# Performance work log

Measured on AMD Instinct MI355X. Metric: run time of the kernel, lower is better.

Reference implementation:

```python
import jax, jax.numpy as jnp
import numpy as np

DIM = 768; HEADS = 12; DIM_HEAD = 64; INNER = HEADS * DIM_HEAD
GT_HEADS = 8; GT_DH = 64; GT_INNER = GT_HEADS * GT_DH
W = 128; DEPTH = 4; NUM_TOKENS = 32000; SEQ = 4096; MAX_SEQ = 4096; B = 1
FF_MULT = 4


def layer_norm(x, g, b, eps=1e-5):
    mu = x.mean(-1, keepdims=True)
    var = ((x - mu) ** 2).mean(-1, keepdims=True)
    return (x - mu) / jnp.sqrt(var + eps) * g + b


def ffn(x, w1_, b1_, w2_, b2_):
    return jax.nn.gelu(x @ w1_ + b1_, approximate=False) @ w2_ + b2_


def global_attn(g, wqkv, wo_, bo_):
    # full causal MHA over the (few) global tokens
    b, n, _ = g.shape
    q, k, v = jnp.split(g @ wqkv, 3, axis=-1)
    sh = lambda t: t.reshape(b, n, GT_HEADS, GT_DH).transpose(0, 2, 1, 3)  # b h n d
    q, k, v = sh(q), sh(k), sh(v)
    sim = jnp.einsum('bhid,bhjd->bhij', q, k) * (GT_DH ** -0.5)
    cm = jnp.triu(jnp.ones((n, n), dtype=bool), k=1)
    sim = jnp.where(cm, -jnp.finfo(sim.dtype).max, sim)
    attn = jax.nn.softmax(sim, axis=-1)
    out = jnp.einsum('bhij,bhjd->bhid', attn, v)
    out = out.transpose(0, 2, 1, 3).reshape(b, n, GT_INNER)
    return out @ wo_ + bo_


def local_attn(x, g, wq_, wkv_, wo_, bo_):
    # windowed look-back attention + global-token keys. n assumed multiple of W.
    b, n, _ = x.shape
    bh = b * HEADS
    buckets = n // W
    sh = lambda t, m: t.reshape(b, m, HEADS, DIM_HEAD).transpose(0, 2, 1, 3).reshape(bh, m, DIM_HEAD)
    q = sh(x @ wq_, n)
    k, v = jnp.split(x @ wkv_, 2, axis=-1)
    k, v = sh(k, n), sh(v, n)
    win = lambda t: t.reshape(bh, buckets, W, DIM_HEAD)
    q, k, v = win(q), win(k), win(v)
    kp = jnp.pad(k, ((0, 0), (1, 0), (0, 0), (0, 0)))
    # NOTE: faithfully replicates upstream bug -- the lambda in the torch code
    # builds BOTH k and v from k, so v becomes the k look-back concat too.
    k2 = jnp.concatenate([kp[:, :-1], kp[:, 1:]], axis=2)  # [bh, buckets, 2W, d]
    v2 = k2
    local_j = 2 * W
    # global tokens (last one dropped)
    gt = g[:, :-1]
    ng = gt.shape[1]
    gk, gv = jnp.split(gt @ wkv_, 2, axis=-1)
    gsh = lambda t: t.reshape(b, ng, HEADS, DIM_HEAD).transpose(0, 2, 1, 3).reshape(bh, ng, DIM_HEAD)
    gk = jnp.broadcast_to(gsh(gk)[:, None], (bh, buckets, ng, DIM_HEAD))
    gv = jnp.broadcast_to(gsh(gv)[:, None], (bh, buckets, ng, DIM_HEAD))
    kf = jnp.concatenate([gk, k2], axis=2)
    vf = jnp.concatenate([gv, v2], axis=2)
    sim = jnp.einsum('bwid,bwjd->bwij', q, kf) * (DIM_HEAD ** -0.5)
    mv = -jnp.finfo(sim.dtype).max
    m_local = jnp.triu(jnp.ones((W, local_j), dtype=bool), k=local_j - W + 1)
    m_local = jnp.broadcast_to(m_local[None], (buckets, W, local_j))
    m_glob = jnp.triu(jnp.ones((buckets, ng), dtype=bool), k=ng - W)
    m_glob = jnp.broadcast_to(m_glob[:, None, :], (buckets, W, ng))
    cmask = jnp.concatenate([m_glob, m_local], axis=-1)[None]
    sim = jnp.where(cmask, mv, sim)
    attn = jax.nn.softmax(sim, axis=-1)
    out = jnp.einsum('bwij,bwjd->bwid', attn, vf)
    out = out.reshape(b, HEADS, n, DIM_HEAD).transpose(0, 2, 1, 3).reshape(b, n, INNER)
    return out @ wo_ + bo_


def setup_inputs() -> dict:
    ks = iter(jax.random.split(jax.random.key(0), 64))
    nrm = lambda shape: jax.random.normal(next(ks), shape, jnp.float32) * 0.02
    return {
        'x': jax.random.randint(next(ks), (B, SEQ), 0, NUM_TOKENS),
        'token_emb': nrm((NUM_TOKENS, DIM)),
        'pos_emb': nrm((MAX_SEQ, DIM)),
        'global_pos_emb': nrm((MAX_SEQ // W, DIM)),
        'gt_ln1_g': jnp.ones((DIM,)), 'gt_ln1_b': jnp.zeros((DIM,)),
        'gt_wqkv': nrm((DIM, 3 * GT_INNER)), 'gt_wo': nrm((GT_INNER, DIM)), 'gt_bo': jnp.zeros((DIM,)),
        'gt_ln2_g': jnp.ones((DIM,)), 'gt_ln2_b': jnp.zeros((DIM,)),
        'gt_w1': nrm((DIM, FF_MULT * DIM)), 'gt_b1': jnp.zeros((FF_MULT * DIM,)),
        'gt_w2': nrm((FF_MULT * DIM, DIM)), 'gt_b2': jnp.zeros((DIM,)),
        'ln1_g': jnp.ones((DEPTH, DIM)), 'ln1_b': jnp.zeros((DEPTH, DIM)),
        'wq': nrm((DEPTH, DIM, INNER)), 'wkv': nrm((DEPTH, DIM, 2 * INNER)),
        'wo': nrm((DEPTH, INNER, DIM)), 'bo': jnp.zeros((DEPTH, DIM)),
        'ln2_g': jnp.ones((DEPTH, DIM)), 'ln2_b': jnp.zeros((DEPTH, DIM)),
        'w1': nrm((DEPTH, DIM, FF_MULT * DIM)), 'b1': jnp.zeros((DEPTH, FF_MULT * DIM)),
        'w2': nrm((DEPTH, FF_MULT * DIM, DIM)), 'b2': jnp.zeros((DEPTH, DIM)),
        'f_ln_g': jnp.ones((DIM,)), 'f_ln_b': jnp.zeros((DIM,)),
        'w_logits': nrm((DIM, NUM_TOKENS)), 'b_logits': jnp.zeros((NUM_TOKENS,)),
    }


def reference(x, token_emb, pos_emb, global_pos_emb,
              gt_ln1_g, gt_ln1_b, gt_wqkv, gt_wo, gt_bo,
              gt_ln2_g, gt_ln2_b, gt_w1, gt_b1, gt_w2, gt_b2,
              ln1_g, ln1_b, wq, wkv, wo, bo,
              ln2_g, ln2_b, w1, b1, w2, b2,
              f_ln_g, f_ln_b, w_logits, b_logits):
    b, n = x.shape
    buckets = n // W  # n % W == 0 for chosen shapes -> r = 0 branch
    h = token_emb[x]                                    # [b, n, dim]
    g = h.reshape(b, buckets, W, DIM).mean(axis=2)      # pooled global tokens
    h = h + pos_emb[:n][None]
    g = g + global_pos_emb[:buckets][None]
    for l in range(DEPTH):
        g = g + global_attn(layer_norm(g, gt_ln1_g, gt_ln1_b), gt_wqkv, gt_wo, gt_bo)
        g = g + ffn(layer_norm(g, gt_ln2_g, gt_ln2_b), gt_w1, gt_b1, gt_w2, gt_b2)
        h = h + local_attn(layer_norm(h, ln1_g[l], ln1_b[l]), g, wq[l], wkv[l], wo[l], bo[l])
        h = h + ffn(layer_norm(h, ln2_g[l], ln2_b[l]), w1[l], b1[l], w2[l], b2[l])
    return layer_norm(h, f_ln_g, f_ln_b) @ w_logits + b_logits
```

## Files before the change

kernel.cpp:

```cpp
#include <hip/hip_runtime.h>
#include <hip/hip_bf16.h>


#define DIMM   768
#define SEQLEN 4096
#define NHEADS 12
#define DH     64
#define WWIN   128
#define NBUCK  32
#define NDEPTH 4
#define FFDIM  3072
#define NTOK   32000
#define QKLD   1536
#define NEG_MAX (-3.402823466e38f)

typedef unsigned short u16;
typedef __attribute__((ext_vector_type(8))) short bf16x8;
typedef __attribute__((ext_vector_type(4))) float f32x4;

#define GLOAD16(gp, lp) \
  __builtin_amdgcn_global_load_lds((const __attribute__((address_space(1))) void*)(gp), \
                                   (__attribute__((address_space(3))) void*)(lp), 16, 0, 0)

__device__ __forceinline__ float b2f(u16 u) {
  union { unsigned int i; float f; } c; c.i = ((unsigned int)u) << 16; return c.f;
}

__global__ __launch_bounds__(256) void embed_kernel(
    const int* __restrict__ x, const float* __restrict__ tok,
    const float* __restrict__ pos, float* __restrict__ h) {
  int row = blockIdx.x;
  int t = threadIdx.x;
  int tk = x[row];
  const float* te = tok + (size_t)tk * DIMM;
  const float* pe = pos + (size_t)row * DIMM;
  float* hr = h + (size_t)row * DIMM;
  hr[t]       = te[t]       + pe[t];
  hr[t + 256] = te[t + 256] + pe[t + 256];
  hr[t + 512] = te[t + 512] + pe[t + 512];
}

__global__ __launch_bounds__(256) void ln_kernel(
    const float* __restrict__ in, const float* __restrict__ gam,
    const float* __restrict__ bet, __hip_bfloat16* __restrict__ out) {
  int row = blockIdx.x;
  int t = threadIdx.x;
  const float* xr = in + (size_t)row * DIMM;
  float v0 = xr[t], v1 = xr[t + 256], v2 = xr[t + 512];
  float s  = v0 + v1 + v2;
  float s2 = v0 * v0 + v1 * v1 + v2 * v2;
  #pragma unroll
  for (int o = 32; o > 0; o >>= 1) {
    s  += __shfl_down(s, o);
    s2 += __shfl_down(s2, o);
  }
  __shared__ float red[2][4];
  int wid = t >> 6, lane = t & 63;
  if (lane == 0) { red[0][wid] = s; red[1][wid] = s2; }
  __syncthreads();
  if (t == 0) {
    float ts  = red[0][0] + red[0][1] + red[0][2] + red[0][3];
    float ts2 = red[1][0] + red[1][1] + red[1][2] + red[1][3];
    float mean = ts * (1.0f / DIMM);
    float var  = ts2 * (1.0f / DIMM) - mean * mean;
    red[0][0] = mean;
    red[1][0] = rsqrtf(var + 1e-5f);
  }
  __syncthreads();
  float mean = red[0][0], rstd = red[1][0];
  __hip_bfloat16* orow = out + (size_t)row * DIMM;
  orow[t]       = __float2bfloat16((v0 - mean) * rstd * gam[t]       + bet[t]);
  orow[t + 256] = __float2bfloat16((v1 - mean) * rstd * gam[t + 256] + bet[t + 256]);
  orow[t + 512] = __float2bfloat16((v2 - mean) * rstd * gam[t + 512] + bet[t + 512]);
}

__global__ __launch_bounds__(256) void wprep_kernel(
    const float* __restrict__ src, u16* __restrict__ dst,
    int ldsrc, int Krows, size_t sls, size_t dls) {
  __shared__ float tile[32][33];
  int l = blockIdx.z;
  int n0 = blockIdx.x * 32, k0 = blockIdx.y * 32;
  int tx = threadIdx.x & 31, ty = threadIdx.x >> 5;
  const float* s = src + (size_t)l * sls;
  u16* d = dst + (size_t)l * dls;
  #pragma unroll
  for (int i = 0; i < 4; ++i)
    tile[ty + i * 8][tx] = s[(size_t)(k0 + ty + i * 8) * ldsrc + n0 + tx];
  __syncthreads();
  #pragma unroll
  for (int i = 0; i < 4; ++i) {
    __hip_bfloat16 b = __float2bfloat16(tile[tx][ty + i * 8]);
    d[(size_t)(n0 + ty + i * 8) * Krows + k0 + tx] = *(u16*)&b;
  }
}

template<int TBM>
__global__ __launch_bounds__(256) void gemm_bf16(
    const u16* __restrict__ A, const u16* __restrict__ Bt,
    const float* __restrict__ bias, const float* __restrict__ resid,
    void* __restrict__ Cv, int K, int ldc, int act, int cbf16) {
  constexpr int MFR = TBM / 32;
  __shared__ u16 As[2][TBM * 32];
  __shared__ u16 Bs[2][128 * 32];
  int tid = threadIdx.x;
  int wave = tid >> 6, lane = tid & 63;

  int lin = blockIdx.y * gridDim.x + blockIdx.x;
  int cpx = (gridDim.x * gridDim.y) >> 3;
  int swz = (lin & 7) * cpx + (lin >> 3);
  int by = swz % gridDim.y;
  int bx = swz / gridDim.y;

  int bm = by * TBM, bn = bx * 128;
  int wm = (wave >> 1) * (TBM / 2), wn = (wave & 1) * 64;
  int fr = lane & 15, fq = lane >> 4;

  f32x4 zero = {0.f, 0.f, 0.f, 0.f};
  f32x4 acc[MFR][4];
  #pragma unroll
  for (int i = 0; i < MFR; ++i)
    #pragma unroll
    for (int j = 0; j < 4; ++j) acc[i][j] = zero;

  int r0 = tid >> 2;
  int kb = ((tid & 3) ^ ((r0 >> 1) & 3)) * 8;
  const u16* aptr = A + (size_t)(bm + r0) * K + kb;
  const u16* bptr = Bt + (size_t)(bn + r0) * K + kb;
  int sA = (fq ^ ((fr >> 1) & 3)) * 8;

#define STAGE_TILE(buf) do {                                          \
    char* lA = (char*)(&As[buf][0]) + wave * 1024;                    \
    char* lB = (char*)(&Bs[buf][0]) + wave * 1024;                    \
    GLOAD16(aptr, lA);                                                \
    if constexpr (TBM == 128) GLOAD16(aptr + (size_t)64 * K, lA + 4096); \
    GLOAD16(bptr, lB);                                                \
    GLOAD16(bptr + (size_t)64 * K, lB + 4096);                        \
    aptr += 32; bptr += 32;                                           \
  } while (0)

  int nk = K >> 5;
  STAGE_TILE(0);
  __syncthreads();

  for (int t = 0; t < nk; ++t) {
    int cur = t & 1;
    if (t + 1 < nk) STAGE_TILE(cur ^ 1);
    bf16x8 af[MFR], bfr[4];
    #pragma unroll
    for (int m = 0; m < MFR; ++m)
      af[m] = *(const bf16x8*)&As[cur][(wm + m * 16 + fr) * 32 + sA];
    #pragma unroll
    for (int n = 0; n < 4; ++n)
      bfr[n] = *(const bf16x8*)&Bs[cur][(wn + n * 16 + fr) * 32 + sA];
    #pragma unroll
    for (int m = 0; m < MFR; ++m)
      #pragma unroll
      for (int n = 0; n < 4; ++n)
        acc[m][n] = __builtin_amdgcn_mfma_f32_16x16x32_bf16(af[m], bfr[n], acc[m][n], 0, 0, 0);
    __syncthreads();
  }
#undef STAGE_TILE

  #pragma unroll
  for (int m = 0; m < MFR; ++m) {
    #pragma unroll
    for (int rr = 0; rr < 4; ++rr) {
      int row = bm + wm + m * 16 + fq * 4 + rr;
      #pragma unroll
      for (int n = 0; n < 4; ++n) {
        int col = bn + wn + n * 16 + fr;
        float v = acc[m][n][rr];
        if (bias) v += bias[col];
        if (act) v = 0.5f * v * (1.0f + erff(v * 0.70710678118654752f));
        if (resid) v += resid[(size_t)row * ldc + col];
        if (cbf16) {
          __hip_bfloat16 b = __float2bfloat16(v);
          ((u16*)Cv)[(size_t)row * ldc + col] = *(u16*)&b;
        } else {
          ((float*)Cv)[(size_t)row * ldc + col] = v;
        }
      }
    }
  }
}

__global__ __launch_bounds__(512, 1) void gemm256(
    const u16* __restrict__ A, const u16* __restrict__ Bt,
    const float* __restrict__ bias, float* __restrict__ C, int K, int ldc) {
  __shared__ __align__(16) char GL[131072];
  const int tid = threadIdx.x;
  const int wave = tid >> 6, lane = tid & 63;
  const int fr = lane & 15, fq = lane >> 4;

  int lin = blockIdx.y * gridDim.x + blockIdx.x;
  int cpx = (gridDim.x * gridDim.y) >> 3;
  int swz = (lin & 7) * cpx + (lin >> 3);
  int by = swz % gridDim.y;
  int bx = swz / gridDim.y;

  const int bm = by * 256, bn = bx * 256;
  const int wm = (wave >> 2) * 128, wn = (wave & 3) * 64;

  const int r_in = tid >> 3;
  const int g_log = (tid & 7) ^ (r_in & 7);
  const size_t a_base = (size_t)(bm + r_in) * K + g_log * 8;
  const size_t b_base = (size_t)(bn + r_in) * K + g_log * 8;
  const int lds_st = wave * 1024;

  const int slot0 = ((fq) ^ (fr & 7)) * 16;
  const int slot1 = ((4 + fq) ^ (fr & 7)) * 16;

  f32x4 acc[8][4];
  #pragma unroll
  for (int i = 0; i < 8; ++i)
    #pragma unroll
    for (int j = 0; j < 4; ++j) acc[i][j] = (f32x4){0.f, 0.f, 0.f, 0.f};

  bf16x8 aq[4][2], bp0[2][2], bp1[2][2];

#define STG4(gb, ldsoff) do {                                   \
    const u16* g_ = (gb);                                       \
    GLOAD16(g_,                  GL + (ldsoff) + lds_st);       \
    GLOAD16(g_ + (size_t)64 * K,  GL + (ldsoff) + 8192 + lds_st);  \
    GLOAD16(g_ + (size_t)128 * K, GL + (ldsoff) + 16384 + lds_st); \
    GLOAD16(g_ + (size_t)192 * K, GL + (ldsoff) + 24576 + lds_st); \
  } while (0)

#define RD_AQ(QOFF, c)                                                   \
    _Pragma("unroll") for (int mm = 0; mm < 4; ++mm) {                   \
      const char* p_ = GL + (c) * 32768 + (wm + (QOFF) + mm * 16 + fr) * 128; \
      aq[mm][0] = *(const bf16x8*)(p_ + slot0);                          \
      aq[mm][1] = *(const bf16x8*)(p_ + slot1);                          \
    }
#define RD_BP(BP, NOFF, c)                                               \
    _Pragma("unroll") for (int nn = 0; nn < 2; ++nn) {                   \
      const char* p_ = GL + 65536 + (c) * 32768 + (wn + (NOFF) + nn * 16 + fr) * 128; \
      BP[nn][0] = *(const bf16x8*)(p_ + slot0);                          \
      BP[nn][1] = *(const bf16x8*)(p_ + slot1);                          \
    }
#define MMA8(MB, NB, BP)                                                 \
    _Pragma("unroll") for (int mm = 0; mm < 4; ++mm)                     \
      _Pragma("unroll") for (int nn = 0; nn < 2; ++nn)                   \
        _Pragma("unroll") for (int kk = 0; kk < 2; ++kk)                 \
          acc[(MB) + mm][(NB) + nn] = __builtin_amdgcn_mfma_f32_16x16x32_bf16( \
              aq[mm][kk], BP[nn][kk], acc[(MB) + mm][(NB) + nn], 0, 0, 0);
#define BAR()      __builtin_amdgcn_s_barrier()
#define SBAR()     __builtin_amdgcn_sched_barrier(0)
#define PRIO(x)    __builtin_amdgcn_s_setprio(x)
#define VMDRAIN()  asm volatile("s_waitcnt vmcnt(0)" ::: "memory")

  const int nk = K >> 6;
  STG4(A + a_base, 0);
  STG4(Bt + b_base, 65536);
  VMDRAIN();
  BAR();

  for (int t = 0; t < nk; ++t) {
    const int c = t & 1;
    if (t + 1 < nk) STG4(A + a_base + (size_t)(t + 1) * 64, (c ^ 1) * 32768);
    RD_AQ(0, c); RD_BP(bp0, 0, c);
    BAR();
    PRIO(1); MMA8(0, 0, bp0); PRIO(0);
    SBAR(); BAR();
    if (t + 1 < nk) STG4(Bt + b_base + (size_t)(t + 1) * 64, 65536 + (c ^ 1) * 32768);
    RD_BP(bp1, 32, c);
    BAR();
    PRIO(1); MMA8(0, 2, bp1); PRIO(0);
    SBAR(); BAR();
    RD_AQ(64, c);
    BAR();
    PRIO(1); MMA8(4, 2, bp1); PRIO(0);
    SBAR(); BAR();
    PRIO(1); MMA8(4, 0, bp0); PRIO(0);
    SBAR();
    VMDRAIN();
    BAR();
  }
#undef STG4
#undef RD_AQ
#undef RD_BP
#undef MMA8

  #pragma unroll
  for (int m = 0; m < 8; ++m) {
    #pragma unroll
    for (int rr = 0; rr < 4; ++rr) {
      int row = bm + wm + m * 16 + fq * 4 + rr;
      #pragma unroll
      for (int n = 0; n < 4; ++n) {
        int col = bn + wn + n * 16 + fr;
        C[(size_t)row * ldc + col] = acc[m][n][rr] + bias[col];
      }
    }
  }
}

__global__ __launch_bounds__(256, 1) void attn_mfma(
    const u16* __restrict__ QK, u16* __restrict__ CTX) {
  __shared__ __align__(16) char LDS[131072];
  char* Kl = LDS;
  char* Kt = LDS + 32768;
  const int w = blockIdx.x, hd = blockIdx.y;
  const int tid = threadIdx.x;
  const int wave = tid >> 6, lane = tid & 63;
  const int fr = lane & 15, fq = lane >> 4;
  char* Pw = LDS + 65536 + wave * 16384;

  {
    const int j = tid;
    const int p = (w - 1) * WWIN + j;
    bf16x8 kv[8];
    if (p >= 0) {
      const bf16x8* src = (const bf16x8*)(QK + (size_t)p * QKLD + DIMM + hd * DH);
      #pragma unroll
      for (int g = 0; g < 8; ++g) kv[g] = src[g];
    } else {
      #pragma unroll
      for (int g = 0; g < 8; ++g) kv[g] = (bf16x8){0, 0, 0, 0, 0, 0, 0, 0};
    }
    #pragma unroll
    for (int g = 0; g < 8; ++g)
      *(bf16x8*)(Kl + j * 128 + ((g ^ (j & 7)) * 16)) = kv[g];
    #pragma unroll
    for (int g = 0; g < 8; ++g)
      #pragma unroll
      for (int e = 0; e < 8; ++e) {
        const int d = g * 8 + e;
        *(u16*)(Kt + d * 512 + (((j >> 3) ^ (d & 7)) * 16) + ((j & 7) * 2)) =
            (u16)kv[g][e];
      }
  }

  bf16x8 aq[2][2];
  #pragma unroll
  for (int m = 0; m < 2; ++m)
    #pragma unroll
    for (int kk = 0; kk < 2; ++kk)
      aq[m][kk] = *(const bf16x8*)(QK +
          (size_t)(w * WWIN + wave * 32 + m * 16 + fr) * QKLD + hd * DH + kk * 32 + fq * 8);

  __syncthreads();

  f32x4 sacc[2][16];
  #pragma unroll
  for (int m = 0; m < 2; ++m)
    #pragma unroll
    for (int n = 0; n < 16; ++n) sacc[m][n] = (f32x4){0.f, 0.f, 0.f, 0.f};
  #pragma unroll
  for (int n = 0; n < 16; ++n) {
    #pragma unroll
    for (int kk = 0; kk < 2; ++kk) {
      bf16x8 bk = *(const bf16x8*)(Kl + (n * 16 + fr) * 128 +
                                   (((kk * 4 + fq) ^ (fr & 7)) * 16));
      #pragma unroll
      for (int m = 0; m < 2; ++m)
        sacc[m][n] = __builtin_amdgcn_mfma_f32_16x16x32_bf16(aq[m][kk], bk, sacc[m][n], 0, 0, 0);
    }
  }

  float inv_[2][4];
  #pragma unroll
  for (int m = 0; m < 2; ++m) {
    #pragma unroll
    for (int rr = 0; rr < 4; ++rr) {
      const int r = wave * 32 + m * 16 + fq * 4 + rr;
      float pv[16];
      float mx = NEG_MAX;
      #pragma unroll
      for (int n = 0; n < 16; ++n) {
        const int j = n * 16 + fr;
        float s = sacc[m][n][rr] * 0.125f;
        bool vis = (j <= r + 128);
        pv[n] = vis ? s : NEG_MAX;
        if (vis) mx = fmaxf(mx, s);
      }
      #pragma unroll
      for (int o = 1; o < 16; o <<= 1) mx = fmaxf(mx, __shfl_xor(mx, o));
      float sum = 0.f;
      #pragma unroll
      for (int n = 0; n < 16; ++n) {
        float p = (pv[n] != NEG_MAX) ? __expf(pv[n] - mx) : 0.f;
        pv[n] = p;
        sum += p;
      }
      #pragma unroll
      for (int o = 1; o < 16; o <<= 1) sum += __shfl_xor(sum, o);
      inv_[m][rr] = 1.0f / sum;
      const int rl = m * 16 + fq * 4 + rr;
      #pragma unroll
      for (int n = 0; n < 16; ++n) {
        __hip_bfloat16 b = __float2bfloat16(pv[n]);
        const int gj = n * 2 + (fr >> 3);
        *(u16*)(Pw + rl * 512 + ((gj ^ (rl & 7)) * 16) + ((fr & 7) * 2)) = *(u16*)&b;
      }
    }
  }
  __syncthreads();

  f32x4 oacc[2][4];
  #pragma unroll
  for (int m = 0; m < 2; ++m)
    #pragma unroll
    for (int nd = 0; nd < 4; ++nd) oacc[m][nd] = (f32x4){0.f, 0.f, 0.f, 0.f};
  #pragma unroll
  for (int kc = 0; kc < 8; ++kc) {
    const int slot = ((kc * 4 + fq) ^ (fr & 7)) * 16;
    bf16x8 pa[2];
    #pragma unroll
    for (int m = 0; m < 2; ++m)
      pa[m] = *(const bf16x8*)(Pw + (m * 16 + fr) * 512 + slot);
    #pragma unroll
    for (int nd = 0; nd < 4; ++nd) {
      bf16x8 kb = *(const bf16x8*)(Kt + (nd * 16 + fr) * 512 + slot);
      #pragma unroll
      for (int m = 0; m < 2; ++m)
        oacc[m][nd] = __builtin_amdgcn_mfma_f32_16x16x32_bf16(pa[m], kb, oacc[m][nd], 0, 0, 0);
    }
  }

  #pragma unroll
  for (int m = 0; m < 2; ++m)
    #pragma unroll
    for (int nd = 0; nd < 4; ++nd)
      #pragma unroll
      for (int rr = 0; rr < 4; ++rr) {
        const int row = w * WWIN + wave * 32 + m * 16 + fq * 4 + rr;
        const int col = hd * DH + nd * 16 + fr;
        __hip_bfloat16 b = __float2bfloat16(oacc[m][nd][rr] * inv_[m][rr]);
        CTX[(size_t)row * DIMM + col] = *(u16*)&b;
      }
}

extern "C" void kernel_launch(void* const* d_in, const int* in_sizes, int n_in,
                              void* d_out, int out_size, void* d_ws, size_t ws_size,
                              hipStream_t stream) {
  const int*   x         = (const int*)d_in[0];
  const float* token_emb = (const float*)d_in[1];
  const float* pos_emb   = (const float*)d_in[2];
  const float* ln1_g = (const float*)d_in[15];
  const float* ln1_b = (const float*)d_in[16];
  const float* wq    = (const float*)d_in[17];
  const float* wkv   = (const float*)d_in[18];
  const float* wo    = (const float*)d_in[19];
  const float* bo    = (const float*)d_in[20];
  const float* ln2_g = (const float*)d_in[21];
  const float* ln2_b = (const float*)d_in[22];
  const float* w1    = (const float*)d_in[23];
  const float* b1    = (const float*)d_in[24];
  const float* w2    = (const float*)d_in[25];
  const float* b2    = (const float*)d_in[26];
  const float* f_ln_g = (const float*)d_in[27];
  const float* f_ln_b = (const float*)d_in[28];
  const float* w_logits = (const float*)d_in[29];
  const float* b_logits = (const float*)d_in[30];
  float* out = (float*)d_out;

  char* ob = (char*)d_out;
  float* h    = (float*)(ob + 0);
  u16* qk     = (u16*)(ob + 12582912);
  u16* ctx    = (u16*)(ob + 25165824);
  u16* mid    = (u16*)(ob + 31457280);
  u16* warena = (u16*)(ob + 56623104);
  const size_t WQ_SZ = (size_t)DIMM * DIMM;
  const size_t W1_SZ = (size_t)DIMM * FFDIM;
  const size_t LW = 3 * WQ_SZ + 2 * W1_SZ;
  u16* qkw_t = warena;
  u16* wo_t  = warena + 2 * WQ_SZ;
  u16* w1_t  = warena + 3 * WQ_SZ;
  u16* w2_t  = warena + 3 * WQ_SZ + W1_SZ;

  u16* wlog_t = (u16*)d_ws;
  __hip_bfloat16* lnbuf = (__hip_bfloat16*)((char*)d_ws + 49152000);

  wprep_kernel<<<dim3(24, 24, 4), 256, 0, stream>>>(wq,  qkw_t,         DIMM,   DIMM,  WQ_SZ,   LW);
  wprep_kernel<<<dim3(24, 24, 4), 256, 0, stream>>>(wkv, qkw_t + WQ_SZ, 2*DIMM, DIMM,  2*WQ_SZ, LW);
  wprep_kernel<<<dim3(24, 24, 4), 256, 0, stream>>>(wo,  wo_t,          DIMM,   DIMM,  WQ_SZ,   LW);
  wprep_kernel<<<dim3(96, 24, 4), 256, 0, stream>>>(w1,  w1_t,          FFDIM,  DIMM,  W1_SZ,   LW);
  wprep_kernel<<<dim3(24, 96, 4), 256, 0, stream>>>(w2,  w2_t,          DIMM,   FFDIM, W1_SZ,   LW);
  wprep_kernel<<<dim3(1000, 24, 1), 256, 0, stream>>>(w_logits, wlog_t, NTOK, DIMM, 0, 0);

  embed_kernel<<<SEQLEN, 256, 0, stream>>>(x, token_emb, pos_emb, h);

  for (int l = 0; l < NDEPTH; ++l) {
    ln_kernel<<<SEQLEN, 256, 0, stream>>>(h, ln1_g + l * DIMM, ln1_b + l * DIMM, lnbuf);
    gemm_bf16<64><<<dim3(12, 64), 256, 0, stream>>>(
        (const u16*)lnbuf, qkw_t + l * LW, nullptr, nullptr, qk, DIMM, QKLD, 0, 1);
    attn_mfma<<<dim3(NBUCK, NHEADS), 256, 0, stream>>>(qk, ctx);
    gemm_bf16<64><<<dim3(6, 64), 256, 0, stream>>>(
        ctx, wo_t + l * LW, bo + l * DIMM, h, h, DIMM, DIMM, 0, 0);
    ln_kernel<<<SEQLEN, 256, 0, stream>>>(h, ln2_g + l * DIMM, ln2_b + l * DIMM, lnbuf);
    gemm_bf16<128><<<dim3(24, 32), 256, 0, stream>>>(
        (const u16*)lnbuf, w1_t + l * LW, b1 + l * FFDIM, nullptr, mid, DIMM, FFDIM, 1, 1);
    gemm_bf16<64><<<dim3(6, 64), 256, 0, stream>>>(
        mid, w2_t + l * LW, b2 + l * DIMM, h, h, FFDIM, DIMM, 0, 0);
  }

  ln_kernel<<<SEQLEN, 256, 0, stream>>>(h, f_ln_g, f_ln_b, lnbuf);
  gemm256<<<dim3(NTOK / 256, SEQLEN / 256), 512, 0, stream>>>(
      (const u16*)lnbuf, wlog_t, b_logits, out, DIMM, NTOK);
}
```

Baseline: 1.232 ms.

## Replace templated layer GEMM with 128x128 K64 pipelined MFMA kernel

Swaps the per-layer bf16 GEMM for a new 128x128-tile kernel with a 64-wide K step, XOR-swizzled LDS and double buffering. Global-to-LDS loads for the next tile are interleaved with four MFMA phases, separated by barriers and raised wave priority. The QK, out-projection and W2 GEMMs move from 64-row to 128-row tiles, halving their grid. This aims to cut LDS/barrier overhead per FLOP and overlap loads with math, at the cost of fewer blocks (192 for the N=768 GEMMs) on a large-CU GPU.

```diff
diff --git a/kernel.cpp b/kernel.cpp
--- a/kernel.cpp
+++ b/kernel.cpp
@@ -22,9 +22,10 @@
   __builtin_amdgcn_global_load_lds((const __attribute__((address_space(1))) void*)(gp), \
                                    (__attribute__((address_space(3))) void*)(lp), 16, 0, 0)
 
-__device__ __forceinline__ float b2f(u16 u) {
-  union { unsigned int i; float f; } c; c.i = ((unsigned int)u) << 16; return c.f;
-}
+#define BAR()      __builtin_amdgcn_s_barrier()
+#define SBAR()     __builtin_amdgcn_sched_barrier(0)
+#define PRIO(x)    __builtin_amdgcn_s_setprio(x)
+#define VMDRAIN()  asm volatile("s_waitcnt vmcnt(0)" ::: "memory")
 
 __global__ __launch_bounds__(256) void embed_kernel(
     const int* __restrict__ x, const float* __restrict__ tok,
@@ -94,16 +95,14 @@
   }
 }
 
-template<int TBM>
-__global__ __launch_bounds__(256) void gemm_bf16(
+__global__ __launch_bounds__(256) void gemm128d(
     const u16* __restrict__ A, const u16* __restrict__ Bt,
     const float* __restrict__ bias, const float* __restrict__ resid,
     void* __restrict__ Cv, int K, int ldc, int act, int cbf16) {
-  constexpr int MFR = TBM / 32;
-  __shared__ u16 As[2][TBM * 32];
-  __shared__ u16 Bs[2][128 * 32];
-  int tid = threadIdx.x;
-  int wave = tid >> 6, lane = tid & 63;
+  __shared__ __align__(16) char GL[65536];
+  const int tid = threadIdx.x;
+  const int wave = tid >> 6, lane = tid & 63;
+  const int fr = lane & 15, fq = lane >> 4;
 
   int lin = blockIdx.y * gridDim.x + blockIdx.x;
   int cpx = (gridDim.x * gridDim.y) >> 3;
@@ -111,58 +110,89 @@
   int by = swz % gridDim.y;
   int bx = swz / gridDim.y;
 
-  int bm = by * TBM, bn = bx * 128;
-  int wm = (wave >> 1) * (TBM / 2), wn = (wave & 1) * 64;
-  int fr = lane & 15, fq = lane >> 4;
-
-  f32x4 zero = {0.f, 0.f, 0.f, 0.f};
-  f32x4 acc[MFR][4];
-  #pragma unroll
-  for (int i = 0; i < MFR; ++i)
-    #pragma unroll
-    for (int j = 0; j < 4; ++j) acc[i][j] = zero;
-
-  int r0 = tid >> 2;
-  int kb = ((tid & 3) ^ ((r0 >> 1) & 3)) * 8;
-  const u16* aptr = A + (size_t)(bm + r0) * K + kb;
-  const u16* bptr = Bt + (size_t)(bn + r0) * K + kb;
-  int sA = (fq ^ ((fr >> 1) & 3)) * 8;
-
-#define STAGE_TILE(buf) do {                                          \
-    char* lA = (char*)(&As[buf][0]) + wave * 1024;                    \
-    char* lB = (char*)(&Bs[buf][0]) + wave * 1024;                    \
-    GLOAD16(aptr, lA);                                                \
-    if constexpr (TBM == 128) GLOAD16(aptr + (size_t)64 * K, lA + 4096); \
-    GLOAD16(bptr, lB);                                                \
-    GLOAD16(bptr + (size_t)64 * K, lB + 4096);                        \
-    aptr += 32; bptr += 32;                                           \
-  } while (0)
-
-  int nk = K >> 5;
-  STAGE_TILE(0);
-  __syncthreads();
+  const int bm = by * 128, bn = bx * 128;
+  const int wm = (wave >> 1) * 64, wn = (wave & 1) * 64;
+
+  const int r_in = tid >> 3;
+  const int g_log = (tid & 7) ^ (r_in & 7);
+  const size_t a_base = (size_t)(bm + r_in) * K + g_log * 8;
+  const size_t b_base = (size_t)(bn + r_in) * K + g_log * 8;
+  const int lds_st = wave * 1024;
+
+  const int slot0 = (fq ^ (fr & 7)) * 16;
+  const int slot1 = ((4 + fq) ^ (fr & 7)) * 16;
+
+  f32x4 acc[4][4];
+  #pragma unroll
+  for (int i = 0; i < 4; ++i)
+    #pragma unroll
+    for (int j = 0; j < 4; ++j) acc[i][j] = (f32x4){0.f, 0.f, 0.f, 0.f};
+
+  bf16x8 aq[4][2], bf0[2], bf1[2], bf2[2], bf3[2];
+
+#define STG4A(tt, c) do { const u16* g_ = A + a_base + (size_t)(tt) * 64;   \
+    GLOAD16(g_,                 GL + (c) * 16384 + lds_st);                 \
+    GLOAD16(g_ + (size_t)32 * K, GL + (c) * 16384 + 4096 + lds_st);         \
+    GLOAD16(g_ + (size_t)64 * K, GL + (c) * 16384 + 8192 + lds_st);         \
+    GLOAD16(g_ + (size_t)96 * K, GL + (c) * 16384 + 12288 + lds_st); } while (0)
+#define STG4B(tt, c) do { const u16* g_ = Bt + b_base + (size_t)(tt) * 64;  \
+    GLOAD16(g_,                 GL + 32768 + (c) * 16384 + lds_st);         \
+    GLOAD16(g_ + (size_t)32 * K, GL + 32768 + (c) * 16384 + 4096 + lds_st); \
+    GLOAD16(g_ + (size_t)64 * K, GL + 32768 + (c) * 16384 + 8192 + lds_st); \
+    GLOAD16(g_ + (size_t)96 * K, GL + 32768 + (c) * 16384 + 12288 + lds_st); } while (0)
+#define RD_A(c)                                                             \
+    _Pragma("unroll") for (int mm = 0; mm < 4; ++mm) {                      \
+      const char* p_ = GL + (c) * 16384 + (wm + mm * 16 + fr) * 128;        \
+      aq[mm][0] = *(const bf16x8*)(p_ + slot0);                             \
+      aq[mm][1] = *(const bf16x8*)(p_ + slot1);                             \
+    }
+#define RD_B(BF, NOFF, c) do {                                              \
+      const char* p_ = GL + 32768 + (c) * 16384 + (wn + (NOFF) + fr) * 128; \
+      BF[0] = *(const bf16x8*)(p_ + slot0);                                 \
+      BF[1] = *(const bf16x8*)(p_ + slot1);                                 \
+    } while (0)
+#define MMA4(N, BF)                                                         \
+    _Pragma("unroll") for (int mm = 0; mm < 4; ++mm)                        \
+      _Pragma("unroll") for (int kk = 0; kk < 2; ++kk)                      \
+        acc[mm][N] = __builtin_amdgcn_mfma_f32_16x16x32_bf16(               \
+            aq[mm][kk], BF[kk], acc[mm][N], 0, 0, 0);
+
+  const int nk = K >> 6;
+  STG4A(0, 0);
+  STG4B(0, 0);
+  VMDRAIN();
+  BAR();
 
   for (int t = 0; t < nk; ++t) {
-    int cur = t & 1;
-    if (t + 1 < nk) STAGE_TILE(cur ^ 1);
-    bf16x8 af[MFR], bfr[4];
-    #pragma unroll
-    for (int m = 0; m < MFR; ++m)
-      af[m] = *(const bf16x8*)&As[cur][(wm + m * 16 + fr) * 32 + sA];
-    #pragma unroll
-    for (int n = 0; n < 4; ++n)
-      bfr[n] = *(const bf16x8*)&Bs[cur][(wn + n * 16 + fr) * 32 + sA];
-    #pragma unroll
-    for (int m = 0; m < MFR; ++m)
-      #pragma unroll
-      for (int n = 0; n < 4; ++n)
-        acc[m][n] = __builtin_amdgcn_mfma_f32_16x16x32_bf16(af[m], bfr[n], acc[m][n], 0, 0, 0);
-    __syncthreads();
-  }
-#undef STAGE_TILE
-
-  #pragma unroll
-  for (int m = 0; m < MFR; ++m) {
+    const int c = t & 1;
+    if (t + 1 < nk) STG4A(t + 1, c ^ 1);
+    RD_A(c); RD_B(bf0, 0, c);
+    BAR();
+    PRIO(1); MMA4(0, bf0); PRIO(0);
+    SBAR(); BAR();
+    if (t + 1 < nk) STG4B(t + 1, c ^ 1);
+    RD_B(bf1, 16, c);
+    BAR();
+    PRIO(1); MMA4(1, bf1); PRIO(0);
+    SBAR(); BAR();
+    RD_B(bf2, 32, c);
+    BAR();
+    PRIO(1); MMA4(2, bf2); PRIO(0);
+    SBAR(); BAR();
+    RD_B(bf3, 48, c);
+    PRIO(1); MMA4(3, bf3); PRIO(0);
+    SBAR();
+    VMDRAIN();
+    BAR();
+  }
+#undef STG4A
+#undef STG4B
+#undef RD_A
+#undef RD_B
+#undef MMA4
+
+  #pragma unroll
+  for (int m = 0; m < 4; ++m) {
     #pragma unroll
     for (int rr = 0; rr < 4; ++rr) {
       int row = bm + wm + m * 16 + fq * 4 + rr;
@@ -244,10 +274,6 @@
         _Pragma("unroll") for (int kk = 0; kk < 2; ++kk)                 \
           acc[(MB) + mm][(NB) + nn] = __builtin_amdgcn_mfma_f32_16x16x32_bf16( \
               aq[mm][kk], BP[nn][kk], acc[(MB) + mm][(NB) + nn], 0, 0, 0);
-#define BAR()      __builtin_amdgcn_s_barrier()
-#define SBAR()     __builtin_amdgcn_sched_barrier(0)
-#define PRIO(x)    __builtin_amdgcn_s_setprio(x)
-#define VMDRAIN()  asm volatile("s_waitcnt vmcnt(0)" ::: "memory")
 
   const int nk = K >> 6;
   STG4(A + a_base, 0);
@@ -483,15 +509,15 @@
 
   for (int l = 0; l < NDEPTH; ++l) {
     ln_kernel<<<SEQLEN, 256, 0, stream>>>(h, ln1_g + l * DIMM, ln1_b + l * DIMM, lnbuf);
-    gemm_bf16<64><<<dim3(12, 64), 256, 0, stream>>>(
+    gemm128d<<<dim3(12, 32), 256, 0, stream>>>(
         (const u16*)lnbuf, qkw_t + l * LW, nullptr, nullptr, qk, DIMM, QKLD, 0, 1);
     attn_mfma<<<dim3(NBUCK, NHEADS), 256, 0, stream>>>(qk, ctx);
-    gemm_bf16<64><<<dim3(6, 64), 256, 0, stream>>>(
+    gemm128d<<<dim3(6, 32), 256, 0, stream>>>(
         ctx, wo_t + l * LW, bo + l * DIMM, h, h, DIMM, DIMM, 0, 0);
     ln_kernel<<<SEQLEN, 256, 0, stream>>>(h, ln2_g + l * DIMM, ln2_b + l * DIMM, lnbuf);
-    gemm_bf16<128><<<dim3(24, 32), 256, 0, stream>>>(
+    gemm128d<<<dim3(24, 32), 256, 0, stream>>>(
         (const u16*)lnbuf, w1_t + l * LW, b1 + l * FFDIM, nullptr, mid, DIMM, FFDIM, 1, 1);
-    gemm_bf16<64><<<dim3(6, 64), 256, 0, stream>>>(
+    gemm128d<<<dim3(6, 32), 256, 0, stream>>>(
         mid, w2_t + l * LW, b2 + l * DIMM, h, h, FFDIM, DIMM, 0, 0);
   }
 
```

New measurement: 1.381 ms. 12.2% more time.

## Deepen gemm_bf16 K-tile to 64 with XOR-swizzled LDS and larger QK tile

Applied to the files above, without the earlier changes.

The generic bf16 GEMM now stages 64-wide K slices per iteration instead of 32, using an 8-slot XOR swizzle for the LDS layout. Each barrier therefore covers twice as many MFMAs, which halves loop and synchronisation overhead. The QK projection GEMM switches from 64-row to 128-row tiles, which halves the grid and raises reuse of the B operand. The cost is double the LDS per block and more registers, which can lower occupancy, and the QK launch has fewer blocks (384).

```diff
diff --git a/kernel.cpp b/kernel.cpp
--- a/kernel.cpp
+++ b/kernel.cpp
@@ -22,9 +22,10 @@
   __builtin_amdgcn_global_load_lds((const __attribute__((address_space(1))) void*)(gp), \
                                    (__attribute__((address_space(3))) void*)(lp), 16, 0, 0)
 
-__device__ __forceinline__ float b2f(u16 u) {
-  union { unsigned int i; float f; } c; c.i = ((unsigned int)u) << 16; return c.f;
-}
+#define BAR()      __builtin_amdgcn_s_barrier()
+#define SBAR()     __builtin_amdgcn_sched_barrier(0)
+#define PRIO(x)    __builtin_amdgcn_s_setprio(x)
+#define VMDRAIN()  asm volatile("s_waitcnt vmcnt(0)" ::: "memory")
 
 __global__ __launch_bounds__(256) void embed_kernel(
     const int* __restrict__ x, const float* __restrict__ tok,
@@ -100,10 +101,11 @@
     const float* __restrict__ bias, const float* __restrict__ resid,
     void* __restrict__ Cv, int K, int ldc, int act, int cbf16) {
   constexpr int MFR = TBM / 32;
-  __shared__ u16 As[2][TBM * 32];
-  __shared__ u16 Bs[2][128 * 32];
-  int tid = threadIdx.x;
-  int wave = tid >> 6, lane = tid & 63;
+  __shared__ __align__(16) u16 As[2][TBM * 64];
+  __shared__ __align__(16) u16 Bs[2][128 * 64];
+  const int tid = threadIdx.x;
+  const int wave = tid >> 6, lane = tid & 63;
+  const int fr = lane & 15, fq = lane >> 4;
 
   int lin = blockIdx.y * gridDim.x + blockIdx.x;
   int cpx = (gridDim.x * gridDim.y) >> 3;
@@ -111,52 +113,69 @@
   int by = swz % gridDim.y;
   int bx = swz / gridDim.y;
 
-  int bm = by * TBM, bn = bx * 128;
-  int wm = (wave >> 1) * (TBM / 2), wn = (wave & 1) * 64;
-  int fr = lane & 15, fq = lane >> 4;
-
-  f32x4 zero = {0.f, 0.f, 0.f, 0.f};
+  const int bm = by * TBM, bn = bx * 128;
+  const int wm = (wave >> 1) * (TBM / 2), wn = (wave & 1) * 64;
+
   f32x4 acc[MFR][4];
   #pragma unroll
   for (int i = 0; i < MFR; ++i)
     #pragma unroll
-    for (int j = 0; j < 4; ++j) acc[i][j] = zero;
-
-  int r0 = tid >> 2;
-  int kb = ((tid & 3) ^ ((r0 >> 1) & 3)) * 8;
-  const u16* aptr = A + (size_t)(bm + r0) * K + kb;
-  const u16* bptr = Bt + (size_t)(bn + r0) * K + kb;
-  int sA = (fq ^ ((fr >> 1) & 3)) * 8;
-
-#define STAGE_TILE(buf) do {                                          \
-    char* lA = (char*)(&As[buf][0]) + wave * 1024;                    \
-    char* lB = (char*)(&Bs[buf][0]) + wave * 1024;                    \
-    GLOAD16(aptr, lA);                                                \
-    if constexpr (TBM == 128) GLOAD16(aptr + (size_t)64 * K, lA + 4096); \
-    GLOAD16(bptr, lB);                                                \
-    GLOAD16(bptr + (size_t)64 * K, lB + 4096);                        \
-    aptr += 32; bptr += 32;                                           \
+    for (int j = 0; j < 4; ++j) acc[i][j] = (f32x4){0.f, 0.f, 0.f, 0.f};
+
+  const int r_in = tid >> 3;
+  const int g_log = (tid & 7) ^ (r_in & 7);
+  const size_t a_base = (size_t)(bm + r_in) * K + g_log * 8;
+  const size_t b_base = (size_t)(bn + r_in) * K + g_log * 8;
+  const int lds_st = wave * 1024;
+
+  const int slot0 = (fq ^ (fr & 7)) * 16;
+  const int slot1 = ((4 + fq) ^ (fr & 7)) * 16;
+
+#define STAGE_TILE(tt, buf) do {                                             \
+    char* lA = (char*)(&As[buf][0]) + lds_st;                                \
+    char* lB = (char*)(&Bs[buf][0]) + lds_st;                                \
+    const u16* ga = A + a_base + (size_t)(tt) * 64;                          \
+    const u16* gb = Bt + b_base + (size_t)(tt) * 64;                         \
+    GLOAD16(ga, lA);                                                         \
+    GLOAD16(ga + (size_t)32 * K, lA + 4096);                                 \
+    if constexpr (TBM == 128) {                                              \
+      GLOAD16(ga + (size_t)64 * K, lA + 8192);                               \
+      GLOAD16(ga + (size_t)96 * K, lA + 12288);                              \
+    }                                                                        \
+    GLOAD16(gb, lB);                                                         \
+    GLOAD16(gb + (size_t)32 * K, lB + 4096);                                 \
+    GLOAD16(gb + (size_t)64 * K, lB + 8192);                                 \
+    GLOAD16(gb + (size_t)96 * K, lB + 12288);                                \
   } while (0)
 
-  int nk = K >> 5;
-  STAGE_TILE(0);
+  const int nk = K >> 6;
+  STAGE_TILE(0, 0);
   __syncthreads();
 
   for (int t = 0; t < nk; ++t) {
-    int cur = t & 1;
-    if (t + 1 < nk) STAGE_TILE(cur ^ 1);
-    bf16x8 af[MFR], bfr[4];
+    const int cur = t & 1;
+    if (t + 1 < nk) STAGE_TILE(t + 1, cur ^ 1);
+    bf16x8 af[MFR][2], bfr[4][2];
+    #pragma unroll
+    for (int m = 0; m < MFR; ++m) {
+      const char* p_ = (const char*)(&As[cur][0]) + (wm + m * 16 + fr) * 128;
+      af[m][0] = *(const bf16x8*)(p_ + slot0);
+      af[m][1] = *(const bf16x8*)(p_ + slot1);
+    }
+    #pragma unroll
+    for (int n = 0; n < 4; ++n) {
+      const char* p_ = (const char*)(&Bs[cur][0]) + (wn + n * 16 + fr) * 128;
+      bfr[n][0] = *(const bf16x8*)(p_ + slot0);
+      bfr[n][1] = *(const bf16x8*)(p_ + slot1);
+    }
     #pragma unroll
     for (int m = 0; m < MFR; ++m)
-      af[m] = *(const bf16x8*)&As[cur][(wm + m * 16 + fr) * 32 + sA];
-    #pragma unroll
-    for (int n = 0; n < 4; ++n)
-      bfr[n] = *(const bf16x8*)&Bs[cur][(wn + n * 16 + fr) * 32 + sA];
-    #pragma unroll
-    for (int m = 0; m < MFR; ++m)
       #pragma unroll
       for (int n = 0; n < 4; ++n)
-        acc[m][n] = __builtin_amdgcn_mfma_f32_16x16x32_bf16(af[m], bfr[n], acc[m][n], 0, 0, 0);
+        #pragma unroll
+        for (int kk = 0; kk < 2; ++kk)
+          acc[m][n] = __builtin_amdgcn_mfma_f32_16x16x32_bf16(
+              af[m][kk], bfr[n][kk], acc[m][n], 0, 0, 0);
     __syncthreads();
   }
 #undef STAGE_TILE
@@ -244,10 +263,6 @@
         _Pragma("unroll") for (int kk = 0; kk < 2; ++kk)                 \
           acc[(MB) + mm][(NB) + nn] = __builtin_amdgcn_mfma_f32_16x16x32_bf16( \
               aq[mm][kk], BP[nn][kk], acc[(MB) + mm][(NB) + nn], 0, 0, 0);
-#define BAR()      __builtin_amdgcn_s_barrier()
-#define SBAR()     __builtin_amdgcn_sched_barrier(0)
-#define PRIO(x)    __builtin_amdgcn_s_setprio(x)
-#define VMDRAIN()  asm volatile("s_waitcnt vmcnt(0)" ::: "memory")
 
   const int nk = K >> 6;
   STG4(A + a_base, 0);
@@ -483,7 +498,7 @@
 
   for (int l = 0; l < NDEPTH; ++l) {
     ln_kernel<<<SEQLEN, 256, 0, stream>>>(h, ln1_g + l * DIMM, ln1_b + l * DIMM, lnbuf);
-    gemm_bf16<64><<<dim3(12, 64), 256, 0, stream>>>(
+    gemm_bf16<128><<<dim3(12, 32), 256, 0, stream>>>(
         (const u16*)lnbuf, qkw_t + l * LW, nullptr, nullptr, qk, DIMM, QKLD, 0, 1);
     attn_mfma<<<dim3(NBUCK, NHEADS), 256, 0, stream>>>(qk, ctx);
     gemm_bf16<64><<<dim3(6, 64), 256, 0, stream>>>(
```

Result: slower. 1.324 ms (+7.5%).
